# Performance work log

Hardware: AMD Instinct MI355X
Metric: run time of the kernel (lower is better)

The kernel has to match this reference:

```python
import jax, jax.numpy as jnp
import numpy as np

B, N, D, H = 16, 8192, 1024, 256


def setup_inputs() -> dict:
    key = jax.random.key(0)
    k1, k2, k3 = jax.random.split(key, 3)
    tiles_embeddings = jax.random.normal(k1, (B, N, D), dtype=jnp.float32)
    # Linear(D -> H, bias=False): weight [H, D]
    W1 = jax.random.normal(k2, (H, D), dtype=jnp.float32) * (1.0 / np.sqrt(D))
    # Linear(H -> 1, bias=False): weight [1, H]
    W2 = jax.random.normal(k3, (1, H), dtype=jnp.float32) * (1.0 / np.sqrt(H))
    return {"tiles_embeddings": tiles_embeddings, "W1": W1, "W2": W2}


def reference(tiles_embeddings, W1, W2):
    # attention MLP: Linear -> Tanh -> Linear (no biases)
    h = jnp.tanh(jnp.einsum("bnd,hd->bnh", tiles_embeddings, W1))   # [B, N, H]
    scores = jnp.einsum("bnh,h->bn", h, W2[0])                       # [B, N]
    attn = jax.nn.softmax(scores, axis=-1)                           # softmax over tiles
    out = jnp.einsum("bn,bnd->bd", attn, tiles_embeddings)           # [B, D]
    return out
```

## Files before the change

### kernel.cpp

```cpp
#include <hip/hip_runtime.h>
#include <hip/hip_bf16.h>
#include <stdint.h>

#define Bn 16
#define Nn 8192
#define Dn 1024
#define Hn 256

typedef __attribute__((ext_vector_type(8))) short bf16x8;
typedef __attribute__((ext_vector_type(4))) float f32x4;

__device__ __forceinline__ short f2bf(float f) {
    __hip_bfloat16 h = __float2bfloat16(f);
    return *reinterpret_cast<short*>(&h);
}

__device__ __forceinline__ float tanh_fast(float x) {
    float e = __expf(2.0f * x);
    return 1.0f - __fdividef(2.0f, 1.0f + e);
}

__global__ __launch_bounds__(256) void k_cvt_w1(const float* __restrict__ W1,
                                                short* __restrict__ w1s) {
    int i   = blockIdx.x * 256 + threadIdx.x;
    int h   = i >> 7;
    int kk8 = i & 127;
    int p   = kk8 >> 3;
    int c8  = kk8 & 7;
    const float* src = W1 + h * Dn + kk8 * 8;
    bf16x8 pk;
#pragma unroll
    for (int j = 0; j < 8; ++j) pk[j] = f2bf(src[j]);
    char* dst = (char*)w1s + p * 32768 + h * 128 + ((c8 ^ (h & 7)) << 4);
    *(bf16x8*)dst = pk;
}

#define XSTR 72

__global__ __launch_bounds__(512) void k_scores(const float* __restrict__ X,
                                                const short* __restrict__ w1s,
                                                const float* __restrict__ W2,
                                                float* __restrict__ scores) {
    __shared__ short xa[128 * XSTR];
    __shared__ short wb[256 * 64];
    __shared__ float sc[128];

    const int tid  = threadIdx.x;
    const int wave = tid >> 6;
    const int lane = tid & 63;
    const int quad = lane >> 4;
    const int l16  = lane & 15;
    const int wr   = wave >> 2;
    const int wc   = wave & 3;

    const long row0 = (long)blockIdx.x * 128;
    const float* xbase = X + row0 * Dn;

    const int srow = tid >> 2;
    const int sk   = (tid & 3) << 4;

    f32x4 acc[4][4];
#pragma unroll
    for (int mi = 0; mi < 4; ++mi)
#pragma unroll
        for (int ni = 0; ni < 4; ++ni)
            acc[mi][ni] = (f32x4){0.f, 0.f, 0.f, 0.f};

    float w2v[4];
#pragma unroll
    for (int ni = 0; ni < 4; ++ni) w2v[ni] = W2[wc * 64 + ni * 16 + l16];

    for (int k0 = 0; k0 < Dn; k0 += 64) {
        {
            const float* src = xbase + (long)srow * Dn + k0 + sk;
            float4 f0 = *(const float4*)(src);
            float4 f1 = *(const float4*)(src + 4);
            float4 f2 = *(const float4*)(src + 8);
            float4 f3 = *(const float4*)(src + 12);
            bf16x8 p0, p1;
            p0[0] = f2bf(f0.x); p0[1] = f2bf(f0.y); p0[2] = f2bf(f0.z); p0[3] = f2bf(f0.w);
            p0[4] = f2bf(f1.x); p0[5] = f2bf(f1.y); p0[6] = f2bf(f1.z); p0[7] = f2bf(f1.w);
            p1[0] = f2bf(f2.x); p1[1] = f2bf(f2.y); p1[2] = f2bf(f2.z); p1[3] = f2bf(f2.w);
            p1[4] = f2bf(f3.x); p1[5] = f2bf(f3.y); p1[6] = f2bf(f3.z); p1[7] = f2bf(f3.w);
            *(bf16x8*)(&xa[srow * XSTR + sk]) = p0;
            *(bf16x8*)(&xa[srow * XSTR + sk + 8]) = p1;
        }
        {
            const char* wsrc = (const char*)w1s + ((long)k0 << 9);
            char* wdst = (char*)wb;
#pragma unroll
            for (int j = 0; j < 4; ++j)
                __builtin_amdgcn_global_load_lds(
                    (const __attribute__((address_space(1))) unsigned int*)(wsrc + j * 8192 + tid * 16),
                    (__attribute__((address_space(3))) unsigned int*)(wdst + j * 8192 + tid * 16),
                    16, 0, 0);
        }
        __syncthreads();

#pragma unroll
        for (int ks = 0; ks < 2; ++ks) {
            bf16x8 af[4], bq[4];
#pragma unroll
            for (int mi = 0; mi < 4; ++mi)
                af[mi] = *(const bf16x8*)(&xa[(wr * 64 + mi * 16 + l16) * XSTR + ks * 32 + quad * 8]);
#pragma unroll
            for (int ni = 0; ni < 4; ++ni) {
                int rw    = wc * 64 + ni * 16 + l16;
                int byteo = (rw * 128 + ks * 64 + quad * 16) ^ ((rw & 7) << 4);
                bq[ni] = *(const bf16x8*)((const char*)wb + byteo);
            }
#pragma unroll
            for (int mi = 0; mi < 4; ++mi)
#pragma unroll
                for (int ni = 0; ni < 4; ++ni)
                    acc[mi][ni] = __builtin_amdgcn_mfma_f32_16x16x32_bf16(af[mi], bq[ni], acc[mi][ni], 0, 0, 0);
        }
        __syncthreads();
    }

    if (tid < 128) sc[tid] = 0.f;
    __syncthreads();

#pragma unroll
    for (int mi = 0; mi < 4; ++mi) {
#pragma unroll
        for (int r = 0; r < 4; ++r) {
            float p = 0.f;
#pragma unroll
            for (int ni = 0; ni < 4; ++ni)
                p += w2v[ni] * tanh_fast(acc[mi][ni][r]);
            p += __shfl_xor(p, 1);
            p += __shfl_xor(p, 2);
            p += __shfl_xor(p, 4);
            p += __shfl_xor(p, 8);
            if (l16 == 0) atomicAdd(&sc[wr * 64 + mi * 16 + quad * 4 + r], p);
        }
    }
    __syncthreads();
    if (tid < 128) scores[row0 + tid] = sc[tid];
}

__global__ __launch_bounds__(1024) void k_softmax(const float* __restrict__ scores,
                                                  float* __restrict__ attn) {
    const int b   = blockIdx.x;
    const int tid = threadIdx.x;
    const float* s = scores + b * Nn;
    __shared__ float redm[16];
    __shared__ float reds[16];

    float4 v0 = ((const float4*)s)[tid * 2];
    float4 v1 = ((const float4*)s)[tid * 2 + 1];

    float m = fmaxf(fmaxf(fmaxf(v0.x, v0.y), fmaxf(v0.z, v0.w)),
                    fmaxf(fmaxf(v1.x, v1.y), fmaxf(v1.z, v1.w)));
#pragma unroll
    for (int o = 32; o >= 1; o >>= 1) m = fmaxf(m, __shfl_xor(m, o));
    if ((tid & 63) == 0) redm[tid >> 6] = m;
    __syncthreads();
    m = redm[0];
#pragma unroll
    for (int i = 1; i < 16; ++i) m = fmaxf(m, redm[i]);

    float e[8];
    e[0] = __expf(v0.x - m); e[1] = __expf(v0.y - m);
    e[2] = __expf(v0.z - m); e[3] = __expf(v0.w - m);
    e[4] = __expf(v1.x - m); e[5] = __expf(v1.y - m);
    e[6] = __expf(v1.z - m); e[7] = __expf(v1.w - m);
    float sum = ((e[0] + e[1]) + (e[2] + e[3])) + ((e[4] + e[5]) + (e[6] + e[7]));
#pragma unroll
    for (int o = 32; o >= 1; o >>= 1) sum += __shfl_xor(sum, o);
    if ((tid & 63) == 0) reds[tid >> 6] = sum;
    __syncthreads();
    float tot = 0.f;
#pragma unroll
    for (int i = 0; i < 16; ++i) tot += reds[i];
    const float inv = 1.0f / tot;

    float* a = attn + b * Nn;
    float4 o0 = make_float4(e[0] * inv, e[1] * inv, e[2] * inv, e[3] * inv);
    float4 o1 = make_float4(e[4] * inv, e[5] * inv, e[6] * inv, e[7] * inv);
    ((float4*)a)[tid * 2]     = o0;
    ((float4*)a)[tid * 2 + 1] = o1;
}

__global__ __launch_bounds__(256) void k_wsum(const float* __restrict__ X,
                                              const float* __restrict__ attn,
                                              float* __restrict__ part) {
    const int slot = blockIdx.y * 64 + blockIdx.x;
    const int flat = 1023 - slot;
    const int b    = flat >> 6;
    const int c    = flat & 63;
    const int tid  = threadIdx.x;
    __shared__ float a_s[128];
    if (tid < 128) a_s[tid] = attn[b * Nn + c * 128 + tid];
    __syncthreads();

    const float* xp = X + ((long)b * Nn + (long)c * 128) * Dn + tid * 4;
    float4 acc = make_float4(0.f, 0.f, 0.f, 0.f);
#pragma unroll 4
    for (int n = 0; n < 128; ++n) {
        float4 x = *(const float4*)(xp + (long)n * Dn);
        float a = a_s[n];
        acc.x += a * x.x; acc.y += a * x.y; acc.z += a * x.z; acc.w += a * x.w;
    }
    *(float4*)(part + (long)flat * Dn + tid * 4) = acc;
}

__global__ __launch_bounds__(256) void k_reduce(const float* __restrict__ part,
                                                float* __restrict__ out) {
    int i = blockIdx.x * 256 + threadIdx.x;
    int b = i >> 10;
    int d = i & 1023;
    const float* p = part + (long)b * 64 * Dn + d;
    float s = 0.f;
#pragma unroll 8
    for (int c = 0; c < 64; ++c) s += p[c * Dn];
    out[i] = s;
}

extern "C" void kernel_launch(void* const* d_in, const int* in_sizes, int n_in,
                              void* d_out, int out_size, void* d_ws, size_t ws_size,
                              hipStream_t stream) {
    (void)in_sizes; (void)n_in; (void)ws_size; (void)out_size;
    const float* X  = (const float*)d_in[0];
    const float* W1 = (const float*)d_in[1];
    const float* W2 = (const float*)d_in[2];
    float* out = (float*)d_out;

    char* ws = (char*)d_ws;
    short* w1s    = (short*)ws;
    float* scores = (float*)(ws + (1 << 19));
    float* attn   = (float*)(ws + (2 << 19));
    float* part   = (float*)(ws + (3 << 19));

    k_cvt_w1<<<(Hn * Dn) / 8 / 256, 256, 0, stream>>>(W1, w1s);
    k_scores<<<(Bn * Nn) / 128, 512, 0, stream>>>(X, w1s, W2, scores);
    k_softmax<<<Bn, 1024, 0, stream>>>(scores, attn);
    dim3 g(64, Bn);
    k_wsum<<<g, 256, 0, stream>>>(X, attn, part);
    k_reduce<<<64, 256, 0, stream>>>(part, out);
}
```

Measured before the change: 810.9 us.

## Fuse softmax and weighted sum into score kernel using online-softmax partials

The score kernel now computes a per-block max and exp-sum over its 128 rows, then immediately reads back its 128x1024 fp32 X tile to form an unnormalised weighted partial sum. A new combine kernel merges the 64 partials per batch with flash-style rescaling. This removes the separate softmax and weighted-sum kernels and their launches, and the re-read of X happens right after the GEMM read, when the 512 KB tile may still be in cache. In exchange, k_scores runs a longer tail that may occupy its blocks longer.

```diff
diff --git a/kernel.cpp b/kernel.cpp
--- a/kernel.cpp
+++ b/kernel.cpp
@@ -40,10 +40,12 @@
 __global__ __launch_bounds__(512) void k_scores(const float* __restrict__ X,
                                                 const short* __restrict__ w1s,
                                                 const float* __restrict__ W2,
-                                                float* __restrict__ scores) {
+                                                float2* __restrict__ ml,
+                                                float* __restrict__ partial) {
     __shared__ short xa[128 * XSTR];
     __shared__ short wb[256 * 64];
     __shared__ float sc[128];
+    __shared__ float mred;
 
     const int tid  = threadIdx.x;
     const int wave = tid >> 6;
@@ -137,85 +139,74 @@
         }
     }
     __syncthreads();
-    if (tid < 128) scores[row0 + tid] = sc[tid];
-}
-
-__global__ __launch_bounds__(1024) void k_softmax(const float* __restrict__ scores,
-                                                  float* __restrict__ attn) {
+
+    if (wave == 0) {
+        float v = fmaxf(sc[lane], sc[64 + lane]);
+#pragma unroll
+        for (int o = 32; o >= 1; o >>= 1) v = fmaxf(v, __shfl_xor(v, o));
+        if (lane == 0) mred = v;
+    }
+    __syncthreads();
+    const float m_c = mred;
+    if (tid < 128) sc[tid] = __expf(sc[tid] - m_c);
+    __syncthreads();
+    if (wave == 0) {
+        float s = sc[lane] + sc[64 + lane];
+#pragma unroll
+        for (int o = 32; o >= 1; o >>= 1) s += __shfl_xor(s, o);
+        if (lane == 0) ml[blockIdx.x] = make_float2(m_c, s);
+    }
+
+    {
+        const float* xw = X + row0 * Dn + tid * 2;
+        float2 a0 = make_float2(0.f, 0.f);
+        float2 a1 = make_float2(0.f, 0.f);
+#pragma unroll 4
+        for (int n = 0; n < 128; n += 2) {
+            float p0 = sc[n];
+            float p1 = sc[n + 1];
+            float2 x0 = *(const float2*)(xw + (long)n * Dn);
+            float2 x1 = *(const float2*)(xw + (long)(n + 1) * Dn);
+            a0.x += p0 * x0.x; a0.y += p0 * x0.y;
+            a1.x += p1 * x1.x; a1.y += p1 * x1.y;
+        }
+        float2 r = make_float2(a0.x + a1.x, a0.y + a1.y);
+        *(float2*)(partial + (long)blockIdx.x * Dn + tid * 2) = r;
+    }
+}
+
+__global__ __launch_bounds__(1024) void k_combine(const float* __restrict__ partial,
+                                                  const float2* __restrict__ ml,
+                                                  float* __restrict__ out) {
     const int b   = blockIdx.x;
     const int tid = threadIdx.x;
-    const float* s = scores + b * Nn;
-    __shared__ float redm[16];
-    __shared__ float reds[16];
-
-    float4 v0 = ((const float4*)s)[tid * 2];
-    float4 v1 = ((const float4*)s)[tid * 2 + 1];
-
-    float m = fmaxf(fmaxf(fmaxf(v0.x, v0.y), fmaxf(v0.z, v0.w)),
-                    fmaxf(fmaxf(v1.x, v1.y), fmaxf(v1.z, v1.w)));
-#pragma unroll
-    for (int o = 32; o >= 1; o >>= 1) m = fmaxf(m, __shfl_xor(m, o));
-    if ((tid & 63) == 0) redm[tid >> 6] = m;
-    __syncthreads();
-    m = redm[0];
-#pragma unroll
-    for (int i = 1; i < 16; ++i) m = fmaxf(m, redm[i]);
-
-    float e[8];
-    e[0] = __expf(v0.x - m); e[1] = __expf(v0.y - m);
-    e[2] = __expf(v0.z - m); e[3] = __expf(v0.w - m);
-    e[4] = __expf(v1.x - m); e[5] = __expf(v1.y - m);
-    e[6] = __expf(v1.z - m); e[7] = __expf(v1.w - m);
-    float sum = ((e[0] + e[1]) + (e[2] + e[3])) + ((e[4] + e[5]) + (e[6] + e[7]));
-#pragma unroll
-    for (int o = 32; o >= 1; o >>= 1) sum += __shfl_xor(sum, o);
-    if ((tid & 63) == 0) reds[tid >> 6] = sum;
-    __syncthreads();
-    float tot = 0.f;
-#pragma unroll
-    for (int i = 0; i < 16; ++i) tot += reds[i];
-    const float inv = 1.0f / tot;
-
-    float* a = attn + b * Nn;
-    float4 o0 = make_float4(e[0] * inv, e[1] * inv, e[2] * inv, e[3] * inv);
-    float4 o1 = make_float4(e[4] * inv, e[5] * inv, e[6] * inv, e[7] * inv);
-    ((float4*)a)[tid * 2]     = o0;
-    ((float4*)a)[tid * 2 + 1] = o1;
-}
-
-__global__ __launch_bounds__(256) void k_wsum(const float* __restrict__ X,
-                                              const float* __restrict__ attn,
-                                              float* __restrict__ part) {
-    const int slot = blockIdx.y * 64 + blockIdx.x;
-    const int flat = 1023 - slot;
-    const int b    = flat >> 6;
-    const int c    = flat & 63;
-    const int tid  = threadIdx.x;
-    __shared__ float a_s[128];
-    if (tid < 128) a_s[tid] = attn[b * Nn + c * 128 + tid];
-    __syncthreads();
-
-    const float* xp = X + ((long)b * Nn + (long)c * 128) * Dn + tid * 4;
-    float4 acc = make_float4(0.f, 0.f, 0.f, 0.f);
-#pragma unroll 4
-    for (int n = 0; n < 128; ++n) {
-        float4 x = *(const float4*)(xp + (long)n * Dn);
-        float a = a_s[n];
-        acc.x += a * x.x; acc.y += a * x.y; acc.z += a * x.z; acc.w += a * x.w;
-    }
-    *(float4*)(part + (long)flat * Dn + tid * 4) = acc;
-}
-
-__global__ __launch_bounds__(256) void k_reduce(const float* __restrict__ part,
-                                                float* __restrict__ out) {
-    int i = blockIdx.x * 256 + threadIdx.x;
-    int b = i >> 10;
-    int d = i & 1023;
-    const float* p = part + (long)b * 64 * Dn + d;
-    float s = 0.f;
+    __shared__ float ms[64];
+    __shared__ float ls[64];
+    __shared__ float es[64];
+
+    if (tid < 64) {
+        float2 v = ml[b * 64 + tid];
+        ms[tid] = v.x;
+        ls[tid] = v.y;
+    }
+    __syncthreads();
+
+    float M = -1e30f;
+#pragma unroll
+    for (int c = 0; c < 64; ++c) M = fmaxf(M, ms[c]);
+    if (tid < 64) es[tid] = __expf(ms[tid] - M);
+    __syncthreads();
+
+    float L = 0.f;
+#pragma unroll
+    for (int c = 0; c < 64; ++c) L += es[c] * ls[c];
+
+    const float* p = partial + (long)b * 64 * Dn + tid;
+    float acc = 0.f;
 #pragma unroll 8
-    for (int c = 0; c < 64; ++c) s += p[c * Dn];
-    out[i] = s;
+    for (int c = 0; c < 64; ++c) acc += es[c] * p[(long)c * Dn];
+
+    out[b * Dn + tid] = acc / L;
 }
 
 extern "C" void kernel_launch(void* const* d_in, const int* in_sizes, int n_in,
@@ -228,15 +219,11 @@
     float* out = (float*)d_out;
 
     char* ws = (char*)d_ws;
-    short* w1s    = (short*)ws;
-    float* scores = (float*)(ws + (1 << 19));
-    float* attn   = (float*)(ws + (2 << 19));
-    float* part   = (float*)(ws + (3 << 19));
+    short*  w1s     = (short*)ws;
+    float2* ml      = (float2*)(ws + (1 << 19));
+    float*  partial = (float*)(ws + (1 << 20));
 
     k_cvt_w1<<<(Hn * Dn) / 8 / 256, 256, 0, stream>>>(W1, w1s);
-    k_scores<<<(Bn * Nn) / 128, 512, 0, stream>>>(X, w1s, W2, scores);
-    k_softmax<<<Bn, 1024, 0, stream>>>(scores, attn);
-    dim3 g(64, Bn);
-    k_wsum<<<g, 256, 0, stream>>>(X, attn, part);
-    k_reduce<<<64, 256, 0, stream>>>(part, out);
-}
+    k_scores<<<(Bn * Nn) / 128, 512, 0, stream>>>(X, w1s, W2, ml, partial);
+    k_combine<<<Bn, 1024, 0, stream>>>(partial, ml, out);
+}
```

Measured after the change: 801.0 us. No clear change (-1.2%).

## Halve score GEMM row tile to 64, drop wsum block reversal, double its chunk

Applied to the files above, without the earlier changes.

The score kernel now processes 64 rows per block with 4 waves, each covering all 64 rows and a 64-column slice of H. This doubles the grid and lowers LDS use, so more blocks can reside per CU, but W1 is reloaded into LDS once per 64 rows instead of once per 128. The weighted-sum kernel now handles 256 rows per block and keeps two interleaved accumulators to expose more independent loads. It also drops the reversed block ordering, which was probably meant to reuse X rows still in cache from the score kernel. k_reduce sums 32 partials instead of 64 to match.

```diff
diff --git a/kernel.cpp b/kernel.cpp
--- a/kernel.cpp
+++ b/kernel.cpp
@@ -37,23 +37,21 @@
 
 #define XSTR 72
 
-__global__ __launch_bounds__(512) void k_scores(const float* __restrict__ X,
+__global__ __launch_bounds__(256) void k_scores(const float* __restrict__ X,
                                                 const short* __restrict__ w1s,
                                                 const float* __restrict__ W2,
                                                 float* __restrict__ scores) {
-    __shared__ short xa[128 * XSTR];
+    __shared__ short xa[64 * XSTR];
     __shared__ short wb[256 * 64];
-    __shared__ float sc[128];
+    __shared__ float sc[64];
 
     const int tid  = threadIdx.x;
     const int wave = tid >> 6;
     const int lane = tid & 63;
     const int quad = lane >> 4;
     const int l16  = lane & 15;
-    const int wr   = wave >> 2;
-    const int wc   = wave & 3;
-
-    const long row0 = (long)blockIdx.x * 128;
+
+    const long row0 = (long)blockIdx.x * 64;
     const float* xbase = X + row0 * Dn;
 
     const int srow = tid >> 2;
@@ -68,7 +66,7 @@
 
     float w2v[4];
 #pragma unroll
-    for (int ni = 0; ni < 4; ++ni) w2v[ni] = W2[wc * 64 + ni * 16 + l16];
+    for (int ni = 0; ni < 4; ++ni) w2v[ni] = W2[wave * 64 + ni * 16 + l16];
 
     for (int k0 = 0; k0 < Dn; k0 += 64) {
         {
@@ -89,10 +87,10 @@
             const char* wsrc = (const char*)w1s + ((long)k0 << 9);
             char* wdst = (char*)wb;
 #pragma unroll
-            for (int j = 0; j < 4; ++j)
+            for (int j = 0; j < 8; ++j)
                 __builtin_amdgcn_global_load_lds(
-                    (const __attribute__((address_space(1))) unsigned int*)(wsrc + j * 8192 + tid * 16),
-                    (__attribute__((address_space(3))) unsigned int*)(wdst + j * 8192 + tid * 16),
+                    (const __attribute__((address_space(1))) unsigned int*)(wsrc + j * 4096 + tid * 16),
+                    (__attribute__((address_space(3))) unsigned int*)(wdst + j * 4096 + tid * 16),
                     16, 0, 0);
         }
         __syncthreads();
@@ -102,10 +100,10 @@
             bf16x8 af[4], bq[4];
 #pragma unroll
             for (int mi = 0; mi < 4; ++mi)
-                af[mi] = *(const bf16x8*)(&xa[(wr * 64 + mi * 16 + l16) * XSTR + ks * 32 + quad * 8]);
+                af[mi] = *(const bf16x8*)(&xa[(mi * 16 + l16) * XSTR + ks * 32 + quad * 8]);
 #pragma unroll
             for (int ni = 0; ni < 4; ++ni) {
-                int rw    = wc * 64 + ni * 16 + l16;
+                int rw    = wave * 64 + ni * 16 + l16;
                 int byteo = (rw * 128 + ks * 64 + quad * 16) ^ ((rw & 7) << 4);
                 bq[ni] = *(const bf16x8*)((const char*)wb + byteo);
             }
@@ -118,7 +116,7 @@
         __syncthreads();
     }
 
-    if (tid < 128) sc[tid] = 0.f;
+    if (tid < 64) sc[tid] = 0.f;
     __syncthreads();
 
 #pragma unroll
@@ -133,11 +131,11 @@
             p += __shfl_xor(p, 2);
             p += __shfl_xor(p, 4);
             p += __shfl_xor(p, 8);
-            if (l16 == 0) atomicAdd(&sc[wr * 64 + mi * 16 + quad * 4 + r], p);
+            if (l16 == 0) atomicAdd(&sc[mi * 16 + quad * 4 + r], p);
         }
     }
     __syncthreads();
-    if (tid < 128) scores[row0 + tid] = sc[tid];
+    if (tid < 64) scores[row0 + tid] = sc[tid];
 }
 
 __global__ __launch_bounds__(1024) void k_softmax(const float* __restrict__ scores,
@@ -177,33 +175,34 @@
     const float inv = 1.0f / tot;
 
     float* a = attn + b * Nn;
-    float4 o0 = make_float4(e[0] * inv, e[1] * inv, e[2] * inv, e[3] * inv);
-    float4 o1 = make_float4(e[4] * inv, e[5] * inv, e[6] * inv, e[7] * inv);
-    ((float4*)a)[tid * 2]     = o0;
-    ((float4*)a)[tid * 2 + 1] = o1;
+    ((float4*)a)[tid * 2]     = make_float4(e[0] * inv, e[1] * inv, e[2] * inv, e[3] * inv);
+    ((float4*)a)[tid * 2 + 1] = make_float4(e[4] * inv, e[5] * inv, e[6] * inv, e[7] * inv);
 }
 
 __global__ __launch_bounds__(256) void k_wsum(const float* __restrict__ X,
                                               const float* __restrict__ attn,
                                               float* __restrict__ part) {
-    const int slot = blockIdx.y * 64 + blockIdx.x;
-    const int flat = 1023 - slot;
-    const int b    = flat >> 6;
-    const int c    = flat & 63;
-    const int tid  = threadIdx.x;
-    __shared__ float a_s[128];
-    if (tid < 128) a_s[tid] = attn[b * Nn + c * 128 + tid];
-    __syncthreads();
-
-    const float* xp = X + ((long)b * Nn + (long)c * 128) * Dn + tid * 4;
-    float4 acc = make_float4(0.f, 0.f, 0.f, 0.f);
+    const int b   = blockIdx.y;
+    const int c   = blockIdx.x;
+    const int tid = threadIdx.x;
+    __shared__ float a_s[256];
+    a_s[tid] = attn[b * Nn + c * 256 + tid];
+    __syncthreads();
+
+    const float* xp = X + ((long)b * Nn + (long)c * 256) * Dn + tid * 4;
+    float4 e = make_float4(0.f, 0.f, 0.f, 0.f);
+    float4 o = make_float4(0.f, 0.f, 0.f, 0.f);
 #pragma unroll 4
-    for (int n = 0; n < 128; ++n) {
-        float4 x = *(const float4*)(xp + (long)n * Dn);
-        float a = a_s[n];
-        acc.x += a * x.x; acc.y += a * x.y; acc.z += a * x.z; acc.w += a * x.w;
+    for (int n = 0; n < 256; n += 2) {
+        float4 x0 = *(const float4*)(xp + (long)n * Dn);
+        float4 x1 = *(const float4*)(xp + (long)(n + 1) * Dn);
+        float a0 = a_s[n];
+        float a1 = a_s[n + 1];
+        e.x += a0 * x0.x; e.y += a0 * x0.y; e.z += a0 * x0.z; e.w += a0 * x0.w;
+        o.x += a1 * x1.x; o.y += a1 * x1.y; o.z += a1 * x1.z; o.w += a1 * x1.w;
     }
-    *(float4*)(part + (long)flat * Dn + tid * 4) = acc;
+    float4 r = make_float4(e.x + o.x, e.y + o.y, e.z + o.z, e.w + o.w);
+    *(float4*)(part + (long)(b * 32 + c) * Dn + tid * 4) = r;
 }
 
 __global__ __launch_bounds__(256) void k_reduce(const float* __restrict__ part,
@@ -211,10 +210,10 @@
     int i = blockIdx.x * 256 + threadIdx.x;
     int b = i >> 10;
     int d = i & 1023;
-    const float* p = part + (long)b * 64 * Dn + d;
+    const float* p = part + (long)b * 32 * Dn + d;
     float s = 0.f;
 #pragma unroll 8
-    for (int c = 0; c < 64; ++c) s += p[c * Dn];
+    for (int c = 0; c < 32; ++c) s += p[c * Dn];
     out[i] = s;
 }
 
@@ -234,9 +233,9 @@
     float* part   = (float*)(ws + (3 << 19));
 
     k_cvt_w1<<<(Hn * Dn) / 8 / 256, 256, 0, stream>>>(W1, w1s);
-    k_scores<<<(Bn * Nn) / 128, 512, 0, stream>>>(X, w1s, W2, scores);
+    k_scores<<<(Bn * Nn) / 64, 256, 0, stream>>>(X, w1s, W2, scores);
     k_softmax<<<Bn, 1024, 0, stream>>>(scores, attn);
-    dim3 g(64, Bn);
+    dim3 g(32, Bn);
     k_wsum<<<g, 256, 0, stream>>>(X, attn, part);
     k_reduce<<<64, 256, 0, stream>>>(part, out);
 }
```

Measured after the change: 817.4 us. No clear change (+0.8%).
